# Kernel tuning notes

Measured on AMD Instinct MI355X. Metric: run time of the kernel, lower is better.

The kernel has to match this reference:

```python
import jax, jax.numpy as jnp
import numpy as np

WS, SHIFT, HEADS = 8, 4, 12
B, H0, W0, C, HID = 16, 64, 64, 384, 1536
EPS = 1e-5


def _rel_pos_index():
    # WindowMSA.double_step_seq(2*Ww-1, Wh, 1, Ww), then coords + coords.T, then flip(1)
    seq1 = np.arange(0, (2 * WS - 1) * WS, 2 * WS - 1)
    seq2 = np.arange(0, WS)
    coords = (seq1[:, None] + seq2[None, :]).reshape(1, -1)  # (1, N)
    idx = coords + coords.T                                   # (N, N)
    return np.ascontiguousarray(idx[:, ::-1]).reshape(-1)

REL_IDX = jnp.asarray(_rel_pos_index())


def _attn_mask(Hp, Wp):
    # Swin shift mask: region labels -> per-window pairwise (-100 where regions differ)
    img = np.zeros((Hp, Wp))
    sl = (slice(0, -WS), slice(-WS, -SHIFT), slice(-SHIFT, None))
    cnt = 0
    for hs in sl:
        for ws in sl:
            img[hs, ws] = cnt
            cnt += 1
    mw = img.reshape(Hp // WS, WS, Wp // WS, WS).transpose(0, 2, 1, 3).reshape(-1, WS * WS)
    am = mw[:, None, :] - mw[:, :, None]
    return jnp.asarray(np.where(am != 0, -100.0, 0.0), np.float32)


def _ln(z, g, b):
    m = z.mean(-1, keepdims=True)
    v = ((z - m) ** 2).mean(-1, keepdims=True)
    return (z - m) * jax.lax.rsqrt(v + EPS) * g + b


def _bn(z, g, b):
    # eval-mode BatchNorm2d with running mean=0, var=1
    scale = g * (1.0 / np.sqrt(1.0 + EPS))
    return z * scale[None, :, None, None] + b[None, :, None, None]


def setup_inputs() -> dict:
    key = jax.random.key(0)
    ks = jax.random.split(key, 8)
    p = lambda k, sh: jax.random.normal(k, sh, jnp.float32) * 0.02
    return {
        "x": jax.random.normal(ks[0], (B, H0 * W0, C), jnp.float32),
        "H": H0, "W": W0,
        "ln1_g": jnp.ones((C,), jnp.float32), "ln1_b": jnp.zeros((C,), jnp.float32),
        "qkv_w": p(ks[1], (3 * C, C)), "qkv_b": jnp.zeros((3 * C,), jnp.float32),
        "rpb_table": p(ks[2], ((2 * WS - 1) ** 2, HEADS)),
        "proj_w": p(ks[3], (C, C)), "proj_b": jnp.zeros((C,), jnp.float32),
        "ln2_g": jnp.ones((C,), jnp.float32), "ln2_b": jnp.zeros((C,), jnp.float32),
        "fc1_w": p(ks[4], (HID, C)), "fc1_b": jnp.zeros((HID,), jnp.float32),
        "bn1_g": jnp.ones((HID,), jnp.float32), "bn1_b": jnp.zeros((HID,), jnp.float32),
        "dw_w": p(ks[5], (HID, 1, 3, 3)), "dw_b": jnp.zeros((HID,), jnp.float32),
        "bn2_g": jnp.ones((HID,), jnp.float32), "bn2_b": jnp.zeros((HID,), jnp.float32),
        "fc2_w": p(ks[6], (C, HID)), "fc2_b": jnp.zeros((C,), jnp.float32),
        "bn3_g": jnp.ones((C,), jnp.float32), "bn3_b": jnp.zeros((C,), jnp.float32),
    }


def reference(x, H, W, ln1_g, ln1_b, qkv_w, qkv_b, rpb_table, proj_w, proj_b,
              ln2_g, ln2_b, fc1_w, fc1_b, bn1_g, bn1_b, dw_w, dw_b,
              bn2_g, bn2_b, fc2_w, fc2_b, bn3_g, bn3_b):
    Bx, L, Cx = x.shape
    hd = Cx // HEADS
    # ---------- shifted-window MHSA branch ----------
    h = _ln(x, ln1_g, ln1_b).reshape(Bx, H, W, Cx)
    h = jnp.roll(h, (-SHIFT, -SHIFT), axis=(1, 2))
    nH, nW = H // WS, W // WS
    N = WS * WS
    win = h.reshape(Bx, nH, WS, nW, WS, Cx).transpose(0, 1, 3, 2, 4, 5).reshape(-1, N, Cx)
    qkv = (win @ qkv_w.T + qkv_b).reshape(-1, N, 3, HEADS, hd).transpose(2, 0, 3, 1, 4)
    q, k, v = qkv[0] * (hd ** -0.5), qkv[1], qkv[2]  # (B*nW, heads, N, hd)
    attn = jnp.einsum('whnd,whmd->whnm', q, k)
    bias = rpb_table[REL_IDX].reshape(N, N, HEADS).transpose(2, 0, 1)  # (heads, N, N)
    attn = attn + bias[None]
    mask = _attn_mask(H, W)  # (num_windows, N, N)
    attn = attn.reshape(Bx, nH * nW, HEADS, N, N) + mask[None, :, None]
    attn = jax.nn.softmax(attn.reshape(-1, HEADS, N, N), axis=-1)
    out = jnp.einsum('whnm,whmd->whnd', attn, v).transpose(0, 2, 1, 3).reshape(-1, N, Cx)
    out = out @ proj_w.T + proj_b
    out = out.reshape(Bx, nH, nW, WS, WS, Cx).transpose(0, 1, 3, 2, 4, 5).reshape(Bx, H, W, Cx)
    out = jnp.roll(out, (SHIFT, SHIFT), axis=(1, 2)).reshape(Bx, L, Cx)
    x = x + out
    # ---------- MlpDWBN branch ----------
    h = _ln(x, ln2_g, ln2_b)
    z = h.transpose(0, 2, 1).reshape(Bx, Cx, H, W)
    z = jnp.einsum('oc,bchw->bohw', fc1_w, z) + fc1_b[None, :, None, None]
    z = jax.nn.gelu(_bn(z, bn1_g, bn1_b), approximate=False)
    z = jax.lax.conv_general_dilated(z, dw_w, (1, 1), 'SAME',
                                     feature_group_count=z.shape[1],
                                     dimension_numbers=('NCHW', 'OIHW', 'NCHW'))
    z = z + dw_b[None, :, None, None]
    z = jax.nn.gelu(_bn(z, bn2_g, bn2_b), approximate=False)
    z = jnp.einsum('oc,bchw->bohw', fc2_w, z) + fc2_b[None, :, None, None]
    z = jax.nn.gelu(_bn(z, bn3_g, bn3_b), approximate=False)
    z = z.reshape(Bx, Cx, -1).transpose(0, 2, 1)
    return x + z
```

## Files before the change

kernel.cpp:

```cpp
#include <hip/hip_runtime.h>
#include <cstddef>


#define CCH 384
#define HIDCH 1536

typedef __attribute__((ext_vector_type(8))) short short8;
typedef __attribute__((ext_vector_type(4))) float f32x4;

__device__ __forceinline__ float gelu_exact(float v) {
  return 0.5f * v * (1.0f + erff(v * 0.70710678118654752440f));
}
__device__ __forceinline__ unsigned short f2bf(float f) {
  unsigned u = __builtin_bit_cast(unsigned, f);
  u = (u + 0x7FFF + ((u >> 16) & 1)) >> 16;
  return (unsigned short)u;
}
__device__ __forceinline__ float bf2f(unsigned short s) {
  return __builtin_bit_cast(float, (unsigned)s << 16);
}
__device__ __forceinline__ int region_label(int p) {
  return (p < 56) ? 0 : ((p < 60) ? 1 : 2);
}

__device__ __forceinline__ void gl_lds16(const void* g, void* l) {
  __builtin_amdgcn_global_load_lds(
      (const __attribute__((address_space(1))) unsigned int*)g,
      (__attribute__((address_space(3))) unsigned int*)l, 16, 0, 0);
}

__global__ __launch_bounds__(256) void convw_kernel(
    const float* __restrict__ a, const float* __restrict__ b,
    const float* __restrict__ c, const float* __restrict__ d,
    const float* __restrict__ dww, unsigned short* __restrict__ o,
    float* __restrict__ dwt) {
  const int i = blockIdx.x * 256 + threadIdx.x;
  if (i < 1769472) {
    float v;
    if (i < 442368) v = a[i];
    else if (i < 589824) v = b[i - 442368];
    else if (i < 1179648) v = c[i - 589824];
    else v = d[i - 1179648];
    o[i] = f2bf(v);
  } else if (i < 1769472 + 13824) {
    const int j = i - 1769472;
    const int tap = j / 1536;
    const int ch = j - tap * 1536;
    dwt[j] = dww[ch * 9 + tap];
  }
}

template <int REMAP>
__global__ __launch_bounds__(256) void ln_kernel(const float* __restrict__ x,
                                                 const float* __restrict__ g,
                                                 const float* __restrict__ b,
                                                 unsigned short* __restrict__ y) {
  const int t = blockIdx.x * 4 + (threadIdx.x >> 6);
  const int lane = threadIdx.x & 63;
  size_t src;
  if (REMAP) {
    const int widx = t >> 6;
    const int n = t & 63;
    const int bb = widx >> 6;
    const int wh = (widx >> 3) & 7;
    const int ww = widx & 7;
    const int hp = wh * 8 + (n >> 3);
    const int wp = ww * 8 + (n & 7);
    const int hs = (hp + 4) & 63;
    const int wsrc = (wp + 4) & 63;
    src = (size_t)bb * 4096 + hs * 64 + wsrc;
  } else {
    src = (size_t)t;
  }
  const float* xr = x + src * CCH + lane * 6;
  const float2 p0 = *(const float2*)xr;
  const float2 p1 = *(const float2*)(xr + 2);
  const float2 p2 = *(const float2*)(xr + 4);
  float v[6] = {p0.x, p0.y, p1.x, p1.y, p2.x, p2.y};
  float s = 0.f, s2 = 0.f;
#pragma unroll
  for (int j = 0; j < 6; ++j) {
    s += v[j];
    s2 += v[j] * v[j];
  }
#pragma unroll
  for (int o = 1; o < 64; o <<= 1) {
    s += __shfl_xor(s, o);
    s2 += __shfl_xor(s2, o);
  }
  const float mean = s * (1.0f / 384.0f);
  const float var = s2 * (1.0f / 384.0f) - mean * mean;
  const float rstd = rsqrtf(var + 1e-5f);
  const float2 g0 = *(const float2*)(g + lane * 6);
  const float2 g1 = *(const float2*)(g + lane * 6 + 2);
  const float2 g2 = *(const float2*)(g + lane * 6 + 4);
  const float2 b0 = *(const float2*)(b + lane * 6);
  const float2 b1 = *(const float2*)(b + lane * 6 + 2);
  const float2 b2 = *(const float2*)(b + lane * 6 + 4);
  const float gg[6] = {g0.x, g0.y, g1.x, g1.y, g2.x, g2.y};
  const float bv[6] = {b0.x, b0.y, b1.x, b1.y, b2.x, b2.y};
  unsigned pk[3];
#pragma unroll
  for (int i = 0; i < 3; ++i) {
    const float r0 = (v[2 * i] - mean) * rstd * gg[2 * i] + bv[2 * i];
    const float r1 = (v[2 * i + 1] - mean) * rstd * gg[2 * i + 1] + bv[2 * i + 1];
    pk[i] = (unsigned)f2bf(r0) | ((unsigned)f2bf(r1) << 16);
  }
  unsigned* yo = (unsigned*)(y + (size_t)t * CCH + lane * 6);
  yo[0] = pk[0];
  yo[1] = pk[1];
  yo[2] = pk[2];
}

template <int MODE>
__global__ __launch_bounds__(256) void mfma_gemm(
    const unsigned short* __restrict__ A, const unsigned short* __restrict__ W,
    const float* __restrict__ bias, void* __restrict__ CoutV,
    const float* __restrict__ Xres, const float* __restrict__ bng,
    const float* __restrict__ bnb, int N, int K) {
  __shared__ __align__(16) unsigned short As[2][128 * 32];
  __shared__ __align__(16) unsigned short Bs[2][128 * 32];
  const int tid = threadIdx.x;
  const int wave = tid >> 6, lane = tid & 63;
  const int qd = lane >> 4, ln16 = lane & 15;
  const int wm = wave >> 1, wn = wave & 1;
  const int m0 = blockIdx.x * 128;
  const int n0 = blockIdx.y * 128;

  f32x4 acc[4][4];
#pragma unroll
  for (int i = 0; i < 4; ++i)
#pragma unroll
    for (int j = 0; j < 4; ++j) acc[i][j] = (f32x4){0.f, 0.f, 0.f, 0.f};

  const int r = tid >> 2;
  const int cks = ((tid & 3) ^ ((tid >> 3) & 3)) * 8;

  const unsigned short* gA0 = A + (size_t)(m0 + r) * K + cks;
  const unsigned short* gA1 = A + (size_t)(m0 + 64 + r) * K + cks;
  const unsigned short* gB0 = W + (size_t)(n0 + r) * K + cks;
  const unsigned short* gB1 = W + (size_t)(n0 + 64 + r) * K + cks;
  const int lofs = wave * 512;

  const int nt = K >> 5;
  gl_lds16(gA0, &As[0][lofs]);
  gl_lds16(gA1, &As[0][2048 + lofs]);
  gl_lds16(gB0, &Bs[0][lofs]);
  gl_lds16(gB1, &Bs[0][2048 + lofs]);

  const int sA = (qd ^ ((ln16 >> 1) & 3)) * 8;

  int cur = 0;
  for (int t = 0; t < nt; ++t) {
    __builtin_amdgcn_s_barrier();
    __builtin_amdgcn_sched_barrier(0);
    if (t + 1 < nt) {
      const int k1 = (t + 1) * 32;
      const int nb = cur ^ 1;
      gl_lds16(gA0 + k1, &As[nb][lofs]);
      gl_lds16(gA1 + k1, &As[nb][2048 + lofs]);
      gl_lds16(gB0 + k1, &Bs[nb][lofs]);
      gl_lds16(gB1 + k1, &Bs[nb][2048 + lofs]);
      asm volatile("s_waitcnt vmcnt(4)" ::: "memory");
    } else {
      asm volatile("s_waitcnt vmcnt(0)" ::: "memory");
    }
    __builtin_amdgcn_s_barrier();
    __builtin_amdgcn_sched_barrier(0);
    short8 af[4], bfr[4];
#pragma unroll
    for (int mt = 0; mt < 4; ++mt)
      af[mt] = *(const short8*)&As[cur][(wm * 64 + mt * 16 + ln16) * 32 + sA];
#pragma unroll
    for (int nt2 = 0; nt2 < 4; ++nt2)
      bfr[nt2] = *(const short8*)&Bs[cur][(wn * 64 + nt2 * 16 + ln16) * 32 + sA];
#pragma unroll
    for (int mt = 0; mt < 4; ++mt)
#pragma unroll
      for (int nt2 = 0; nt2 < 4; ++nt2)
        acc[mt][nt2] = __builtin_amdgcn_mfma_f32_16x16x32_bf16(
            af[mt], bfr[nt2], acc[mt][nt2], 0, 0, 0);
    cur ^= 1;
  }

  const float RSQ = 0.99999500003749969f;
#pragma unroll
  for (int mt = 0; mt < 4; ++mt) {
#pragma unroll
    for (int nt2 = 0; nt2 < 4; ++nt2) {
      const int col = n0 + wn * 64 + nt2 * 16 + ln16;
      const int rbase = m0 + wm * 64 + mt * 16 + qd * 4;
#pragma unroll
      for (int rg = 0; rg < 4; ++rg) {
        const int row = rbase + rg;
        const float val = acc[mt][nt2][rg] + bias[col];
        if (MODE == 0) {
          ((unsigned short*)CoutV)[(size_t)row * N + col] = f2bf(val);
        } else if (MODE == 1) {
          const int widx = row >> 6, n = row & 63;
          const int bb = widx >> 6, wh = (widx >> 3) & 7, wwi = widx & 7;
          const int hp = wh * 8 + (n >> 3), wp = wwi * 8 + (n & 7);
          const int hh = (hp + 4) & 63, wwp = (wp + 4) & 63;
          const size_t dst = ((size_t)bb * 4096 + hh * 64 + wwp) * CCH + col;
          ((float*)CoutV)[dst] = Xres[dst] + val;
        } else {
          const float vbn = val * (bng[col] * RSQ) + bnb[col];
          const float ge = gelu_exact(vbn);
          if (MODE == 2) {
            ((unsigned short*)CoutV)[(size_t)row * N + col] = f2bf(ge);
          } else {
            float* o = (float*)CoutV + (size_t)row * N + col;
            *o = *o + ge;
          }
        }
      }
    }
  }
}

__global__ __launch_bounds__(256) void attn_kernel(
    const unsigned short* __restrict__ qkv, const float* __restrict__ rpb,
    unsigned short* __restrict__ ao) {
  __shared__ __align__(16) unsigned short Pl[4][64 * 72];
  __shared__ float Inv[4][64];
  const int wloc = blockIdx.x;
  const int wave = threadIdx.x >> 6;
  const int lane = threadIdx.x & 63;
  const int head = blockIdx.y * 4 + wave;
  const int ln16 = lane & 15, qd = lane >> 4;
  const int wpos = wloc & 63;
  const int wh = (wpos >> 3) & 7, ww = wpos & 7;
  const unsigned short* qb = qkv + (size_t)wloc * 64 * 1152 + head * 32;

  short8 aq[4], bk[4];
#pragma unroll
  for (int t = 0; t < 4; ++t) {
    aq[t] = *(const short8*)(qb + (size_t)(t * 16 + ln16) * 1152 + qd * 8);
    bk[t] = *(const short8*)(qb + (size_t)(t * 16 + ln16) * 1152 + 384 + qd * 8);
  }
  short8 av[2][2];
#pragma unroll
  for (int dt = 0; dt < 2; ++dt)
#pragma unroll
    for (int ks = 0; ks < 2; ++ks)
#pragma unroll
      for (int j = 0; j < 8; ++j)
        av[dt][ks][j] = (short)qb[(size_t)(ks * 32 + qd * 8 + j) * 1152 + 768 +
                                  dt * 16 + ln16];

  f32x4 accS[4][4];
#pragma unroll
  for (int i = 0; i < 4; ++i)
#pragma unroll
    for (int j = 0; j < 4; ++j) accS[i][j] = (f32x4){0.f, 0.f, 0.f, 0.f};
#pragma unroll
  for (int mt = 0; mt < 4; ++mt)
#pragma unroll
    for (int nt = 0; nt < 4; ++nt)
      accS[mt][nt] = __builtin_amdgcn_mfma_f32_16x16x32_bf16(
          aq[mt], bk[nt], accS[mt][nt], 0, 0, 0);

  int cmv[4], rlm[4];
#pragma unroll
  for (int nt = 0; nt < 4; ++nt) {
    const int m = nt * 16 + ln16;
    const int mf = 63 - m;
    cmv[nt] = 15 * (mf >> 3) + (mf & 7);
    rlm[nt] =
        region_label(wh * 8 + (m >> 3)) * 3 + region_label(ww * 8 + (m & 7));
  }
  const float scale = 0.17677669529663687f;
  unsigned short* pw = &Pl[wave][0];
#pragma unroll
  for (int mt = 0; mt < 4; ++mt) {
#pragma unroll
    for (int rg = 0; rg < 4; ++rg) {
      const int n = mt * 16 + qd * 4 + rg;
      const int cn = 15 * (n >> 3) + (n & 7);
      const int rln =
          region_label(wh * 8 + (n >> 3)) * 3 + region_label(ww * 8 + (n & 7));
      float vv[4];
#pragma unroll
      for (int nt = 0; nt < 4; ++nt) {
        float sv = accS[mt][nt][rg] * scale + rpb[(cn + cmv[nt]) * 12 + head];
        if (rln != rlm[nt]) sv -= 100.f;
        vv[nt] = sv;
      }
      float mx = fmaxf(fmaxf(vv[0], vv[1]), fmaxf(vv[2], vv[3]));
      mx = fmaxf(mx, __shfl_xor(mx, 1));
      mx = fmaxf(mx, __shfl_xor(mx, 2));
      mx = fmaxf(mx, __shfl_xor(mx, 4));
      mx = fmaxf(mx, __shfl_xor(mx, 8));
      float sum = 0.f;
#pragma unroll
      for (int nt = 0; nt < 4; ++nt) {
        vv[nt] = __expf(vv[nt] - mx);
        sum += vv[nt];
      }
      sum += __shfl_xor(sum, 1);
      sum += __shfl_xor(sum, 2);
      sum += __shfl_xor(sum, 4);
      sum += __shfl_xor(sum, 8);
      if (ln16 == 0) Inv[wave][n] = 1.0f / sum;
#pragma unroll
      for (int nt = 0; nt < 4; ++nt)
        pw[n * 72 + nt * 16 + ln16] = f2bf(vv[nt]);
    }
  }

  f32x4 accO[2][4];
#pragma unroll
  for (int i = 0; i < 2; ++i)
#pragma unroll
    for (int j = 0; j < 4; ++j) accO[i][j] = (f32x4){0.f, 0.f, 0.f, 0.f};
#pragma unroll
  for (int ks = 0; ks < 2; ++ks) {
    short8 pb[4];
#pragma unroll
    for (int ntile = 0; ntile < 4; ++ntile)
      pb[ntile] =
          *(const short8*)&pw[(ntile * 16 + ln16) * 72 + ks * 32 + qd * 8];
#pragma unroll
    for (int dt = 0; dt < 2; ++dt)
#pragma unroll
      for (int ntile = 0; ntile < 4; ++ntile)
        accO[dt][ntile] = __builtin_amdgcn_mfma_f32_16x16x32_bf16(
            av[dt][ks], pb[ntile], accO[dt][ntile], 0, 0, 0);
  }

  float invn[4];
#pragma unroll
  for (int ntile = 0; ntile < 4; ++ntile)
    invn[ntile] = Inv[wave][ntile * 16 + ln16];
#pragma unroll
  for (int dt = 0; dt < 2; ++dt) {
#pragma unroll
    for (int ntile = 0; ntile < 4; ++ntile) {
      const int tok = ntile * 16 + ln16;
      const int d0 = dt * 16 + qd * 4;
      uint2 st;
      st.x = (unsigned)f2bf(accO[dt][ntile][0] * invn[ntile]) |
             ((unsigned)f2bf(accO[dt][ntile][1] * invn[ntile]) << 16);
      st.y = (unsigned)f2bf(accO[dt][ntile][2] * invn[ntile]) |
             ((unsigned)f2bf(accO[dt][ntile][3] * invn[ntile]) << 16);
      *(uint2*)&ao[((size_t)wloc * 64 + tok) * CCH + head * 32 + d0] = st;
    }
  }
}

__global__ __launch_bounds__(256) void dw_kernel(
    const unsigned short* __restrict__ z1, const float* __restrict__ dwt,
    const float* __restrict__ dwb, const float* __restrict__ bn2g,
    const float* __restrict__ bn2b, unsigned short* __restrict__ z2) {
  const int g = blockIdx.x * 256 + threadIdx.x;
  const int pix = g / 192;
  const int cg = g - pix * 192;
  const int c0 = cg * 8;
  const int p = pix & 4095;
  const int h = p >> 6, w = p & 63;
  const unsigned short* zb = z1 + (size_t)(pix >> 12) * 4096 * HIDCH;

  float a[8];
  {
    const float4 b0 = *(const float4*)&dwb[c0];
    const float4 b1 = *(const float4*)&dwb[c0 + 4];
    a[0] = b0.x; a[1] = b0.y; a[2] = b0.z; a[3] = b0.w;
    a[4] = b1.x; a[5] = b1.y; a[6] = b1.z; a[7] = b1.w;
  }
#pragma unroll
  for (int dh = -1; dh <= 1; ++dh) {
    const int hh = h + dh;
    if (hh < 0 || hh > 63) continue;
#pragma unroll
    for (int dx = -1; dx <= 1; ++dx) {
      const int wn = w + dx;
      if (wn < 0 || wn > 63) continue;
      const int tap = (dh + 1) * 3 + (dx + 1);
      const int4 zv = *(const int4*)&zb[((size_t)hh * 64 + wn) * HIDCH + c0];
      const float* wp = &dwt[tap * HIDCH + c0];
      const float4 w0 = *(const float4*)wp;
      const float4 w1 = *(const float4*)(wp + 4);
      a[0] += bf2f((unsigned short)(zv.x & 0xFFFF)) * w0.x;
      a[1] += bf2f((unsigned short)(((unsigned)zv.x) >> 16)) * w0.y;
      a[2] += bf2f((unsigned short)(zv.y & 0xFFFF)) * w0.z;
      a[3] += bf2f((unsigned short)(((unsigned)zv.y) >> 16)) * w0.w;
      a[4] += bf2f((unsigned short)(zv.z & 0xFFFF)) * w1.x;
      a[5] += bf2f((unsigned short)(((unsigned)zv.z) >> 16)) * w1.y;
      a[6] += bf2f((unsigned short)(zv.w & 0xFFFF)) * w1.z;
      a[7] += bf2f((unsigned short)(((unsigned)zv.w) >> 16)) * w1.w;
    }
  }
  const float RSQ = 0.99999500003749969f;
  const float4 g0 = *(const float4*)&bn2g[c0];
  const float4 g1 = *(const float4*)&bn2g[c0 + 4];
  const float4 bb0 = *(const float4*)&bn2b[c0];
  const float4 bb1 = *(const float4*)&bn2b[c0 + 4];
  const float gs[8] = {g0.x, g0.y, g0.z, g0.w, g1.x, g1.y, g1.z, g1.w};
  const float bs[8] = {bb0.x, bb0.y, bb0.z, bb0.w, bb1.x, bb1.y, bb1.z, bb1.w};
  unsigned pk[4];
#pragma unroll
  for (int i = 0; i < 4; ++i) {
    const float v0 = gelu_exact(a[2 * i] * (gs[2 * i] * RSQ) + bs[2 * i]);
    const float v1 =
        gelu_exact(a[2 * i + 1] * (gs[2 * i + 1] * RSQ) + bs[2 * i + 1]);
    pk[i] = (unsigned)f2bf(v0) | ((unsigned)f2bf(v1) << 16);
  }
  int4 st;
  st.x = pk[0]; st.y = pk[1]; st.z = pk[2]; st.w = pk[3];
  *(int4*)&z2[(size_t)pix * HIDCH + c0] = st;
}

extern "C" void kernel_launch(void* const* d_in, const int* in_sizes, int n_in,
                              void* d_out, int out_size, void* d_ws,
                              size_t ws_size, hipStream_t stream) {
  const float* x = (const float*)d_in[0];
  const float* ln1_g = (const float*)d_in[3];
  const float* ln1_b = (const float*)d_in[4];
  const float* qkv_w = (const float*)d_in[5];
  const float* qkv_b = (const float*)d_in[6];
  const float* rpb = (const float*)d_in[7];
  const float* proj_w = (const float*)d_in[8];
  const float* proj_b = (const float*)d_in[9];
  const float* ln2_g = (const float*)d_in[10];
  const float* ln2_b = (const float*)d_in[11];
  const float* fc1_w = (const float*)d_in[12];
  const float* fc1_b = (const float*)d_in[13];
  const float* bn1_g = (const float*)d_in[14];
  const float* bn1_b = (const float*)d_in[15];
  const float* dw_w = (const float*)d_in[16];
  const float* dw_b = (const float*)d_in[17];
  const float* bn2_g = (const float*)d_in[18];
  const float* bn2_b = (const float*)d_in[19];
  const float* fc2_w = (const float*)d_in[20];
  const float* fc2_b = (const float*)d_in[21];
  const float* bn3_g = (const float*)d_in[22];
  const float* bn3_b = (const float*)d_in[23];
  float* out = (float*)d_out;

  char* ws = (char*)d_ws;
  unsigned short* wsA = (unsigned short*)ws;
  unsigned short* wsAO = (unsigned short*)(ws + 50331648);
  unsigned short* wsQ = (unsigned short*)(ws + 100663296);
  unsigned short* wbf = (unsigned short*)(ws + 150994944);
  float* dwt = (float*)(ws + 154533888);
  unsigned short* w_qkv = wbf;
  unsigned short* w_proj = wbf + 442368;
  unsigned short* w_fc1 = wbf + 589824;
  unsigned short* w_fc2 = wbf + 1179648;

  convw_kernel<<<6966, 256, 0, stream>>>(qkv_w, proj_w, fc1_w, fc2_w, dw_w,
                                         wbf, dwt);
  ln_kernel<1><<<16384, 256, 0, stream>>>(x, ln1_g, ln1_b, wsA);
  for (int cb = 0; cb < 4; ++cb) {
    mfma_gemm<0><<<dim3(128, 9), 256, 0, stream>>>(
        wsA + (size_t)cb * 16384 * CCH, w_qkv, qkv_b, wsQ, nullptr, nullptr,
        nullptr, 1152, CCH);
    attn_kernel<<<dim3(256, 3), 256, 0, stream>>>(
        wsQ, rpb, wsAO + (size_t)cb * 16384 * CCH);
  }
  mfma_gemm<1><<<dim3(512, 3), 256, 0, stream>>>(wsAO, w_proj, proj_b, out, x,
                                                 nullptr, nullptr, CCH, CCH);
  ln_kernel<0><<<16384, 256, 0, stream>>>(out, ln2_g, ln2_b, wsA);
  for (int cb = 0; cb < 4; ++cb) {
    mfma_gemm<2><<<dim3(128, 12), 256, 0, stream>>>(
        wsA + (size_t)cb * 16384 * CCH, w_fc1, fc1_b, wsAO, nullptr, bn1_g,
        bn1_b, HIDCH, CCH);
    dw_kernel<<<12288, 256, 0, stream>>>(wsAO, dwt, dw_b, bn2_g, bn2_b, wsQ);
    mfma_gemm<3><<<dim3(128, 3), 256, 0, stream>>>(
        wsQ, w_fc2, fc2_b, out + (size_t)cb * 16384 * CCH, nullptr, bn3_g,
        bn3_b, CCH, HIDCH);
  }
}
```

Baseline: 1.122 ms.

## Use 512-thread GEMM blocks with 2x4 wave grid and XCD-aware block remap

The MFMA GEMM now runs 8 waves per 128x128 tile instead of 4. Each wave computes a 64x32 sub-tile, and every thread issues one async global-to-LDS load per operand per k-step instead of two. Block IDs are also remapped so consecutive logical tiles land on the same XCD (lid%8 grouping), which should improve L2 locality. The aim is better latency hiding and cache reuse, at the cost of less register-level reuse per wave and more LDS fragment reads per MFMA.

```diff
diff --git a/kernel.cpp b/kernel.cpp
--- a/kernel.cpp
+++ b/kernel.cpp
@@ -113,71 +113,74 @@
 }
 
 template <int MODE>
-__global__ __launch_bounds__(256) void mfma_gemm(
+__global__ __launch_bounds__(512) void mfma_gemm(
     const unsigned short* __restrict__ A, const unsigned short* __restrict__ W,
     const float* __restrict__ bias, void* __restrict__ CoutV,
     const float* __restrict__ Xres, const float* __restrict__ bng,
     const float* __restrict__ bnb, int N, int K) {
-  __shared__ __align__(16) unsigned short As[2][128 * 32];
-  __shared__ __align__(16) unsigned short Bs[2][128 * 32];
+  __shared__ __align__(16) char smem[32768];
   const int tid = threadIdx.x;
   const int wave = tid >> 6, lane = tid & 63;
   const int qd = lane >> 4, ln16 = lane & 15;
-  const int wm = wave >> 1, wn = wave & 1;
-  const int m0 = blockIdx.x * 128;
-  const int n0 = blockIdx.y * 128;
-
-  f32x4 acc[4][4];
+  const int wm = wave >> 2, wn = wave & 3;
+
+  const int nx = gridDim.x;
+  const int lid0 = blockIdx.x + blockIdx.y * nx;
+  const int tot = nx * gridDim.y;
+  int lid = lid0;
+  if ((tot & 7) == 0) lid = (lid0 & 7) * (tot >> 3) + (lid0 >> 3);
+  const int m0 = (lid % nx) * 128;
+  const int n0 = (lid / nx) * 128;
+
+  f32x4 acc[4][2];
 #pragma unroll
   for (int i = 0; i < 4; ++i)
 #pragma unroll
-    for (int j = 0; j < 4; ++j) acc[i][j] = (f32x4){0.f, 0.f, 0.f, 0.f};
+    for (int j = 0; j < 2; ++j) acc[i][j] = (f32x4){0.f, 0.f, 0.f, 0.f};
 
   const int r = tid >> 2;
   const int cks = ((tid & 3) ^ ((tid >> 3) & 3)) * 8;
 
-  const unsigned short* gA0 = A + (size_t)(m0 + r) * K + cks;
-  const unsigned short* gA1 = A + (size_t)(m0 + 64 + r) * K + cks;
-  const unsigned short* gB0 = W + (size_t)(n0 + r) * K + cks;
-  const unsigned short* gB1 = W + (size_t)(n0 + 64 + r) * K + cks;
-  const int lofs = wave * 512;
-
-  const int nt = K >> 5;
-  gl_lds16(gA0, &As[0][lofs]);
-  gl_lds16(gA1, &As[0][2048 + lofs]);
-  gl_lds16(gB0, &Bs[0][lofs]);
-  gl_lds16(gB1, &Bs[0][2048 + lofs]);
+  const unsigned short* gA = A + (size_t)(m0 + r) * K + cks;
+  const unsigned short* gB = W + (size_t)(n0 + r) * K + cks;
+  char* baseA = smem;
+  char* baseB = smem + 16384;
+  const int wofs = wave * 1024;
+
+  const int ntk = K >> 5;
+  gl_lds16(gA, baseA + wofs);
+  gl_lds16(gB, baseB + wofs);
 
   const int sA = (qd ^ ((ln16 >> 1) & 3)) * 8;
 
   int cur = 0;
-  for (int t = 0; t < nt; ++t) {
+  for (int t = 0; t < ntk; ++t) {
     __builtin_amdgcn_s_barrier();
     __builtin_amdgcn_sched_barrier(0);
-    if (t + 1 < nt) {
+    if (t + 1 < ntk) {
       const int k1 = (t + 1) * 32;
       const int nb = cur ^ 1;
-      gl_lds16(gA0 + k1, &As[nb][lofs]);
-      gl_lds16(gA1 + k1, &As[nb][2048 + lofs]);
-      gl_lds16(gB0 + k1, &Bs[nb][lofs]);
-      gl_lds16(gB1 + k1, &Bs[nb][2048 + lofs]);
-      asm volatile("s_waitcnt vmcnt(4)" ::: "memory");
+      gl_lds16(gA + k1, baseA + nb * 8192 + wofs);
+      gl_lds16(gB + k1, baseB + nb * 8192 + wofs);
+      asm volatile("s_waitcnt vmcnt(2)" ::: "memory");
     } else {
       asm volatile("s_waitcnt vmcnt(0)" ::: "memory");
     }
     __builtin_amdgcn_s_barrier();
     __builtin_amdgcn_sched_barrier(0);
-    short8 af[4], bfr[4];
+    short8 af[4], bfr[2];
 #pragma unroll
     for (int mt = 0; mt < 4; ++mt)
-      af[mt] = *(const short8*)&As[cur][(wm * 64 + mt * 16 + ln16) * 32 + sA];
-#pragma unroll
-    for (int nt2 = 0; nt2 < 4; ++nt2)
-      bfr[nt2] = *(const short8*)&Bs[cur][(wn * 64 + nt2 * 16 + ln16) * 32 + sA];
+      af[mt] = *(const short8*)(baseA + cur * 8192 +
+                                ((wm * 64 + mt * 16 + ln16) * 32 + sA) * 2);
+#pragma unroll
+    for (int nt2 = 0; nt2 < 2; ++nt2)
+      bfr[nt2] = *(const short8*)(baseB + cur * 8192 +
+                                  ((wn * 32 + nt2 * 16 + ln16) * 32 + sA) * 2);
 #pragma unroll
     for (int mt = 0; mt < 4; ++mt)
 #pragma unroll
-      for (int nt2 = 0; nt2 < 4; ++nt2)
+      for (int nt2 = 0; nt2 < 2; ++nt2)
         acc[mt][nt2] = __builtin_amdgcn_mfma_f32_16x16x32_bf16(
             af[mt], bfr[nt2], acc[mt][nt2], 0, 0, 0);
     cur ^= 1;
@@ -187,8 +190,8 @@
 #pragma unroll
   for (int mt = 0; mt < 4; ++mt) {
 #pragma unroll
-    for (int nt2 = 0; nt2 < 4; ++nt2) {
-      const int col = n0 + wn * 64 + nt2 * 16 + ln16;
+    for (int nt2 = 0; nt2 < 2; ++nt2) {
+      const int col = n0 + wn * 32 + nt2 * 16 + ln16;
       const int rbase = m0 + wm * 64 + mt * 16 + qd * 4;
 #pragma unroll
       for (int rg = 0; rg < 4; ++rg) {
@@ -452,21 +455,21 @@
                                          wbf, dwt);
   ln_kernel<1><<<16384, 256, 0, stream>>>(x, ln1_g, ln1_b, wsA);
   for (int cb = 0; cb < 4; ++cb) {
-    mfma_gemm<0><<<dim3(128, 9), 256, 0, stream>>>(
+    mfma_gemm<0><<<dim3(128, 9), 512, 0, stream>>>(
         wsA + (size_t)cb * 16384 * CCH, w_qkv, qkv_b, wsQ, nullptr, nullptr,
         nullptr, 1152, CCH);
     attn_kernel<<<dim3(256, 3), 256, 0, stream>>>(
         wsQ, rpb, wsAO + (size_t)cb * 16384 * CCH);
   }
-  mfma_gemm<1><<<dim3(512, 3), 256, 0, stream>>>(wsAO, w_proj, proj_b, out, x,
+  mfma_gemm<1><<<dim3(512, 3), 512, 0, stream>>>(wsAO, w_proj, proj_b, out, x,
                                                  nullptr, nullptr, CCH, CCH);
   ln_kernel<0><<<16384, 256, 0, stream>>>(out, ln2_g, ln2_b, wsA);
   for (int cb = 0; cb < 4; ++cb) {
-    mfma_gemm<2><<<dim3(128, 12), 256, 0, stream>>>(
+    mfma_gemm<2><<<dim3(128, 12), 512, 0, stream>>>(
         wsA + (size_t)cb * 16384 * CCH, w_fc1, fc1_b, wsAO, nullptr, bn1_g,
         bn1_b, HIDCH, CCH);
     dw_kernel<<<12288, 256, 0, stream>>>(wsAO, dwt, dw_b, bn2_g, bn2_b, wsQ);
-    mfma_gemm<3><<<dim3(128, 3), 256, 0, stream>>>(
+    mfma_gemm<3><<<dim3(128, 3), 512, 0, stream>>>(
         wsQ, w_fc2, fc2_b, out + (size_t)cb * 16384 * CCH, nullptr, bn3_g,
         bn3_b, CCH, HIDCH);
   }
```

Result: faster. 1.071 ms (-4.5%).
